# Kernel tuning notes

Hardware: AMD Instinct MI355X
Metric: run time of the kernel (lower is better)

## Reference

```python
import jax, jax.numpy as jnp
import numpy as np

B, K, D, H = 16, 256, 256, 128

def setup_inputs() -> dict:
    key = jax.random.key(0)
    k1, k2, k3 = jax.random.split(key, 3)
    x = jax.random.normal(k1, (B, K, D), dtype=jnp.float32)
    # Linear(2D, H): weight stored as (2D, H) for x @ W convention
    W1 = jax.random.normal(k2, (2 * D, H), dtype=jnp.float32) * (1.0 / np.sqrt(2 * D))
    b1 = jnp.zeros((H,), dtype=jnp.float32)
    W2 = jax.random.normal(k3, (H, D), dtype=jnp.float32) * (1.0 / np.sqrt(H))
    b2 = jnp.zeros((D,), dtype=jnp.float32)
    return {"x": x, "W1": W1, "b1": b1, "W2": W2, "b2": b2}

def reference(x, W1, b1, W2, b2):
    # Original: for each i, concat([x_i broadcast, x_j]) -> Linear -> ReLU -> Linear -> mean_j, + residual.
    # Split the first Linear over the concat: W1 = [W1a; W1b], so
    # pre-act(i,j) = x_i @ W1a + x_j @ W1b + b1  (avoids materializing the concat).
    D_ = x.shape[-1]
    W1a, W1b = W1[:D_], W1[D_:]
    a = jnp.einsum('bkd,dh->bkh', x, W1a)            # B x K x H (query side)
    b = jnp.einsum('bkd,dh->bkh', x, W1b)            # B x K x H (key side)
    h = jax.nn.relu(a[:, :, None, :] + b[:, None, :, :] + b1)  # B x K x K x H
    mh = h.mean(axis=2)                               # mean over j; Linear commutes with mean
    out = jnp.einsum('bkh,hd->bkd', mh, W2) + b2      # B x K x D
    return out + x
```

## Files before the change

kernel.cpp:

```cpp
#include <hip/hip_runtime.h>

typedef __attribute__((ext_vector_type(8))) short bf16x8;
typedef __attribute__((ext_vector_type(4))) float f32x4;

union FragU { uint4 q; bf16x8 h; };

__device__ __forceinline__ unsigned short f2bf(float f) {
  unsigned u = __float_as_uint(f);
  u += 0x7FFFu + ((u >> 16) & 1u);
  return (unsigned short)(u >> 16);
}
__device__ __forceinline__ unsigned pack2(float lo, float hi) {
  return (unsigned)f2bf(lo) | ((unsigned)f2bf(hi) << 16);
}

__global__ __launch_bounds__(256) void kX(
    const float* __restrict__ x, const float* __restrict__ W1,
    const float* __restrict__ W2, uint4* __restrict__ xbf,
    uint4* __restrict__ w1f, uint4* __restrict__ w2f)
{
  const int u = blockIdx.x * 256 + threadIdx.x;
  if (u < 131072) {
    const int l = u & 63, c = (u >> 6) & 7, t = (u >> 9) & 15, b = u >> 13;
    const int fr = l & 15, fq = l >> 4;
    const float* p = x + (size_t)((b * 16 + t) * 16 + fr) * 256 + c * 32 + fq * 8;
    float4 va = *(const float4*)p;
    float4 vb = *(const float4*)(p + 4);
    xbf[u] = make_uint4(pack2(va.x, va.y), pack2(va.z, va.w),
                        pack2(vb.x, vb.y), pack2(vb.z, vb.w));
  } else if (u < 139264) {
    const int u2 = u - 131072;
    const int l = u2 & 63, c = (u2 >> 6) & 7, hc = u2 >> 9;
    const int fr = l & 15, fq = l >> 4;
    const float* p = W1 + (size_t)((fr >= 8) ? 256 : 0) * 128 +
                     (size_t)(c * 32 + fq * 8) * 128 + hc * 8 + (fr & 7);
    float v[8];
#pragma unroll
    for (int j = 0; j < 8; ++j) v[j] = p[(size_t)j * 128];
    w1f[u2] = make_uint4(pack2(v[0], v[1]), pack2(v[2], v[3]),
                         pack2(v[4], v[5]), pack2(v[6], v[7]));
  } else if (u < 143360) {
    const int u3 = u - 139264;
    const int l = u3 & 63, c = (u3 >> 6) & 3, dg = u3 >> 8;
    const int fr = l & 15, fq = l >> 4;
    const float* p = W2 + (size_t)(c * 32 + fq * 8) * 256 + dg * 16 + fr;
    float v[8];
#pragma unroll
    for (int j = 0; j < 8; ++j) v[j] = p[(size_t)j * 256];
    w2f[u3] = make_uint4(pack2(v[0], v[1]), pack2(v[2], v[3]),
                         pack2(v[4], v[5]), pack2(v[6], v[7]));
  }
}

__global__ __launch_bounds__(1024) void kA(
    const uint4* __restrict__ xbf, const uint4* __restrict__ w1f,
    const float* __restrict__ b1, uint4* __restrict__ mf)
{
  __shared__ float Cs[8][260];
  __shared__ float As[8][260];
  __shared__ float sortedC[8][256];
  __shared__ float sufS[8][260];

  const int tid = threadIdx.x, lane = tid & 63, wv = tid >> 6;
  const int b = blockIdx.x, hc = blockIdx.y;
  const int fr = lane & 15, fq = lane >> 4;

  FragU afr[8];
#pragma unroll
  for (int c = 0; c < 8; ++c) afr[c].q = w1f[(hc * 8 + c) * 64 + lane];

  float b1v[4];
#pragma unroll
  for (int g = 0; g < 4; ++g)
    b1v[g] = (fq >= 2) ? b1[hc * 8 + (fq - 2) * 4 + g] : 0.f;

  {
    const int t = wv;
    f32x4 acc = {0.f, 0.f, 0.f, 0.f};
#pragma unroll
    for (int c = 0; c < 8; ++c) {
      FragU bfr;
      bfr.q = xbf[((size_t)(b * 16 + t) * 8 + c) * 64 + lane];
      acc = __builtin_amdgcn_mfma_f32_16x16x32_bf16(afr[c].h, bfr.h, acc, 0, 0, 0);
    }
    const int m = t * 16 + fr;
    if (fq < 2) {
#pragma unroll
      for (int g = 0; g < 4; ++g) As[fq * 4 + g][m] = acc[g];
    } else {
#pragma unroll
      for (int g = 0; g < 4; ++g) Cs[(fq - 2) * 4 + g][m] = acc[g] + b1v[g];
    }
  }
  __syncthreads();

  if (wv < 8) {
    const int hp = wv;
    float v0 = Cs[hp][lane * 4 + 0], v1 = Cs[hp][lane * 4 + 1];
    float v2 = Cs[hp][lane * 4 + 2], v3 = Cs[hp][lane * 4 + 3];

#define CE2(X, Y, UP)                                     \
    {                                                     \
      float mn = fminf(X, Y), mx = fmaxf(X, Y);           \
      X = (UP) ? mn : mx;  Y = (UP) ? mx : mn;            \
    }
    CE2(v0, v1, true) CE2(v2, v3, false)
    {
      const bool up4 = (lane & 1) == 0;
      CE2(v0, v2, up4) CE2(v1, v3, up4)
      CE2(v0, v1, up4) CE2(v2, v3, up4)
    }
#pragma unroll
    for (int k4 = 2; k4 <= 64; k4 <<= 1) {
      const bool up = (lane & k4) == 0;
#pragma unroll
      for (int j4 = k4 >> 1; j4 >= 1; j4 >>= 1) {
        const bool keepMin = (((lane & j4) == 0) == up);
#define CEX(V)                                            \
        {                                                 \
          float o = __shfl_xor(V, j4, 64);                \
          V = keepMin ? fminf(V, o) : fmaxf(V, o);        \
        }
        CEX(v0) CEX(v1) CEX(v2) CEX(v3)
#undef CEX
      }
      CE2(v0, v2, up) CE2(v1, v3, up)
      CE2(v0, v1, up) CE2(v2, v3, up)
    }
#undef CE2

    const float sl = (v0 + v1) + (v2 + v3);
    float inc = sl;
#pragma unroll
    for (int off = 1; off < 64; off <<= 1) {
      float t = __shfl_down(inc, off, 64);
      inc += (lane + off < 64) ? t : 0.f;
    }
    const float T = inc - sl;
    const float su3 = T + v3;
    const float su2 = su3 + v2;
    const float su1 = su2 + v1;
    const float su0 = su1 + v0;
    sortedC[hp][lane * 4 + 0] = v0;
    sortedC[hp][lane * 4 + 1] = v1;
    sortedC[hp][lane * 4 + 2] = v2;
    sortedC[hp][lane * 4 + 3] = v3;
    sufS[hp][lane * 4 + 0] = su0;
    sufS[hp][lane * 4 + 1] = su1;
    sufS[hp][lane * 4 + 2] = su2;
    sufS[hp][lane * 4 + 3] = su3;
    if (lane == 0) sufS[hp][256] = 0.f;
  }
  __syncthreads();

  {
    const int hp = wv & 7, half = wv >> 3;
#pragma unroll
    for (int q = 0; q < 2; ++q) {
      const int m = half * 128 + q * 64 + lane;
      const float a = As[hp][m];
      const float t = -a;
      int idx = 0;
#pragma unroll
      for (int st = 128; st >= 1; st >>= 1)
        idx += (sortedC[hp][idx + st - 1] <= t) ? st : 0;
      const float cnt = (float)(256 - idx);
      const float S = sufS[hp][idx];
      As[hp][m] = (cnt * a + S) * (1.f / 256.f);
    }
  }
  __syncthreads();

  if (tid < 256) {
    const int fr2 = tid & 15, T2 = tid >> 4;
    uint4 o = make_uint4(pack2(As[0][tid], As[1][tid]), pack2(As[2][tid], As[3][tid]),
                         pack2(As[4][tid], As[5][tid]), pack2(As[6][tid], As[7][tid]));
    mf[((size_t)(b * 16 + T2) * 4 + (hc >> 2)) * 64 + (hc & 3) * 16 + fr2] = o;
  }
}

__global__ __launch_bounds__(256) void kB(
    const uint4* __restrict__ mf, const uint4* __restrict__ w2f,
    const float* __restrict__ b2, const float* __restrict__ x,
    float* __restrict__ out)
{
  const int tid = threadIdx.x, lane = tid & 63, wu = tid >> 6;
  const int mt = blockIdx.x;
  const int dg = blockIdx.y * 4 + wu;
  const int fr = lane & 15, fq = lane >> 4;

  f32x4 acc = {0.f, 0.f, 0.f, 0.f};
#pragma unroll
  for (int c = 0; c < 4; ++c) {
    FragU a, bb;
    a.q  = mf[((size_t)mt * 4 + c) * 64 + lane];
    bb.q = w2f[((size_t)dg * 4 + c) * 64 + lane];
    acc = __builtin_amdgcn_mfma_f32_16x16x32_bf16(a.h, bb.h, acc, 0, 0, 0);
  }

  const int d = dg * 16 + fr;
  const float bv = b2[d];
#pragma unroll
  for (int g = 0; g < 4; ++g) {
    const int m = mt * 16 + fq * 4 + g;
    const size_t o = (size_t)m * 256 + d;
    out[o] = acc[g] + bv + x[o];
  }
}

extern "C" void kernel_launch(void* const* d_in, const int* in_sizes, int n_in,
                              void* d_out, int out_size, void* d_ws, size_t ws_size,
                              hipStream_t stream) {
  const float* x  = (const float*)d_in[0];
  const float* W1 = (const float*)d_in[1];
  const float* b1 = (const float*)d_in[2];
  const float* W2 = (const float*)d_in[3];
  const float* b2 = (const float*)d_in[4];
  float* out = (float*)d_out;

  char* ws = (char*)d_ws;
  uint4* xbf = (uint4*)ws;
  uint4* w1f = (uint4*)(ws + (2u << 20));
  uint4* w2f = (uint4*)(ws + (2u << 20) + (128u << 10));
  uint4* mf  = (uint4*)(ws + (2u << 20) + (192u << 10));

  kX<<<560, 256, 0, stream>>>(x, W1, W2, xbf, w1f, w2f);
  kA<<<dim3(16, 16), 1024, 0, stream>>>(xbf, w1f, b1, mf);
  kB<<<dim3(256, 4), 256, 0, stream>>>(mf, w2f, b2, x, out);
}
```

Measured before the change: 21.50 us.

## Replace per-element binary search with pivot count plus leaf scan in kA

In kA, the 8-step binary search over 256 sorted values and the full suffix-sum array are replaced by a two-level lookup. Each thread counts against 16 block pivots held in registers, reads one per-block suffix sum, then linearly scans a 16-element leaf in shared memory. kA also moves to 512 threads, with each wave doing two MFMA tiles and four queries, and every thread takes part in a narrower uint2 output write. kX and kB are relaunched with 1024-thread blocks, fewer of them, aiming to cut dependent LDS latency and launch/block overhead at the cost of more ALU compares per query.

```diff
diff --git a/kernel.cpp b/kernel.cpp
--- a/kernel.cpp
+++ b/kernel.cpp
@@ -14,12 +14,12 @@
   return (unsigned)f2bf(lo) | ((unsigned)f2bf(hi) << 16);
 }
 
-__global__ __launch_bounds__(256) void kX(
+__global__ __launch_bounds__(1024) void kX(
     const float* __restrict__ x, const float* __restrict__ W1,
     const float* __restrict__ W2, uint4* __restrict__ xbf,
     uint4* __restrict__ w1f, uint4* __restrict__ w2f)
 {
-  const int u = blockIdx.x * 256 + threadIdx.x;
+  const int u = blockIdx.x * 1024 + threadIdx.x;
   if (u < 131072) {
     const int l = u & 63, c = (u >> 6) & 7, t = (u >> 9) & 15, b = u >> 13;
     const int fr = l & 15, fq = l >> 4;
@@ -52,14 +52,15 @@
   }
 }
 
-__global__ __launch_bounds__(1024) void kA(
+__global__ __launch_bounds__(512) void kA(
     const uint4* __restrict__ xbf, const uint4* __restrict__ w1f,
     const float* __restrict__ b1, uint4* __restrict__ mf)
 {
   __shared__ float Cs[8][260];
   __shared__ float As[8][260];
   __shared__ float sortedC[8][256];
-  __shared__ float sufS[8][260];
+  __shared__ float Piv[8][16];
+  __shared__ float sufBlk[8][16];
 
   const int tid = threadIdx.x, lane = tid & 63, wv = tid >> 6;
   const int b = blockIdx.x, hc = blockIdx.y;
@@ -74,8 +75,9 @@
   for (int g = 0; g < 4; ++g)
     b1v[g] = (fq >= 2) ? b1[hc * 8 + (fq - 2) * 4 + g] : 0.f;
 
-  {
-    const int t = wv;
+#pragma unroll
+  for (int s = 0; s < 2; ++s) {
+    const int t = wv + s * 8;
     f32x4 acc = {0.f, 0.f, 0.f, 0.f};
 #pragma unroll
     for (int c = 0; c < 8; ++c) {
@@ -94,7 +96,7 @@
   }
   __syncthreads();
 
-  if (wv < 8) {
+  {
     const int hp = wv;
     float v0 = Cs[hp][lane * 4 + 0], v1 = Cs[hp][lane * 4 + 1];
     float v2 = Cs[hp][lane * 4 + 2], v3 = Cs[hp][lane * 4 + 3];
@@ -145,48 +147,64 @@
     sortedC[hp][lane * 4 + 1] = v1;
     sortedC[hp][lane * 4 + 2] = v2;
     sortedC[hp][lane * 4 + 3] = v3;
-    sufS[hp][lane * 4 + 0] = su0;
-    sufS[hp][lane * 4 + 1] = su1;
-    sufS[hp][lane * 4 + 2] = su2;
-    sufS[hp][lane * 4 + 3] = su3;
-    if (lane == 0) sufS[hp][256] = 0.f;
+    if ((lane & 3) == 3) Piv[hp][lane >> 2] = v3;
+    if ((lane & 3) == 0 && lane) sufBlk[hp][(lane >> 2) - 1] = su0;
+    if (lane == 0) sufBlk[hp][15] = 0.f;
   }
   __syncthreads();
 
   {
-    const int hp = wv & 7, half = wv >> 3;
-#pragma unroll
-    for (int q = 0; q < 2; ++q) {
-      const int m = half * 128 + q * 64 + lane;
+    const int hp = wv;
+    float piv[16];
+#pragma unroll
+    for (int j = 0; j < 16; j += 4) {
+      float4 pv = *(const float4*)&Piv[hp][j];
+      piv[j] = pv.x; piv[j + 1] = pv.y; piv[j + 2] = pv.z; piv[j + 3] = pv.w;
+    }
+#pragma unroll
+    for (int q = 0; q < 4; ++q) {
+      const int m = q * 64 + lane;
       const float a = As[hp][m];
       const float t = -a;
-      int idx = 0;
-#pragma unroll
-      for (int st = 128; st >= 1; st >>= 1)
-        idx += (sortedC[hp][idx + st - 1] <= t) ? st : 0;
-      const float cnt = (float)(256 - idx);
-      const float S = sufS[hp][idx];
-      As[hp][m] = (cnt * a + S) * (1.f / 256.f);
+      int p = 0;
+#pragma unroll
+      for (int j = 0; j < 16; ++j) p += (piv[j] <= t) ? 1 : 0;
+      p = (p > 15) ? 15 : p;
+      const float Sb = sufBlk[hp][p];
+      const float* leafp = &sortedC[hp][p * 16];
+      float sumL = 0.f; int cntL = 0;
+#pragma unroll
+      for (int j = 0; j < 16; j += 4) {
+        float4 lv = *(const float4*)&leafp[j];
+        if (lv.x > t) { sumL += lv.x; ++cntL; }
+        if (lv.y > t) { sumL += lv.y; ++cntL; }
+        if (lv.z > t) { sumL += lv.z; ++cntL; }
+        if (lv.w > t) { sumL += lv.w; ++cntL; }
+      }
+      const float cnt = (float)(240 - 16 * p + cntL);
+      As[hp][m] = (cnt * a + (Sb + sumL)) * (1.f / 256.f);
     }
   }
   __syncthreads();
 
-  if (tid < 256) {
-    const int fr2 = tid & 15, T2 = tid >> 4;
-    uint4 o = make_uint4(pack2(As[0][tid], As[1][tid]), pack2(As[2][tid], As[3][tid]),
-                         pack2(As[4][tid], As[5][tid]), pack2(As[6][tid], As[7][tid]));
-    mf[((size_t)(b * 16 + T2) * 4 + (hc >> 2)) * 64 + (hc & 3) * 16 + fr2] = o;
-  }
-}
-
-__global__ __launch_bounds__(256) void kB(
+  {
+    const int m = tid >> 1, half = tid & 1, j0 = half * 4;
+    const int fr2 = m & 15, T2 = m >> 4;
+    uint2 o = make_uint2(pack2(As[j0][m], As[j0 + 1][m]),
+                         pack2(As[j0 + 2][m], As[j0 + 3][m]));
+    const size_t unit = ((size_t)(b * 16 + T2) * 4 + (hc >> 2)) * 64 + (hc & 3) * 16 + fr2;
+    *(uint2*)((unsigned*)mf + unit * 4 + half * 2) = o;
+  }
+}
+
+__global__ __launch_bounds__(1024) void kB(
     const uint4* __restrict__ mf, const uint4* __restrict__ w2f,
     const float* __restrict__ b2, const float* __restrict__ x,
     float* __restrict__ out)
 {
   const int tid = threadIdx.x, lane = tid & 63, wu = tid >> 6;
   const int mt = blockIdx.x;
-  const int dg = blockIdx.y * 4 + wu;
+  const int dg = wu;
   const int fr = lane & 15, fq = lane >> 4;
 
   f32x4 acc = {0.f, 0.f, 0.f, 0.f};
@@ -224,7 +242,7 @@
   uint4* w2f = (uint4*)(ws + (2u << 20) + (128u << 10));
   uint4* mf  = (uint4*)(ws + (2u << 20) + (192u << 10));
 
-  kX<<<560, 256, 0, stream>>>(x, W1, W2, xbf, w1f, w2f);
-  kA<<<dim3(16, 16), 1024, 0, stream>>>(xbf, w1f, b1, mf);
-  kB<<<dim3(256, 4), 256, 0, stream>>>(mf, w2f, b2, x, out);
-}
+  kX<<<140, 1024, 0, stream>>>(x, W1, W2, xbf, w1f, w2f);
+  kA<<<dim3(16, 16), 512, 0, stream>>>(xbf, w1f, b1, mf);
+  kB<<<256, 1024, 0, stream>>>(mf, w2f, b2, x, out);
+}
```

Result: no change. 21.85 us (+1.6%).

## Fuse weight bf16 packing into consumers and split sort into two half-sorts

Applied to the files above, without the earlier changes.

Weight conversion to bf16 fragments moves out of the prep kernel and into kA and kB, which now read fp32 W1/W2 directly and pack them in registers. The sort of the C column now uses all 16 waves, each sorting 128 values. The ReLU-mean lookup becomes a two-level search (pivot count, then a 16-element leaf scan) across both sorted halves, replacing the binary search over one full sort. kB now runs one 1024-thread block per row tile. The aim is a shorter serial sort stage and less prep work, at the cost of redundant strided weight loads in every block.

```diff
diff --git a/kernel.cpp b/kernel.cpp
--- a/kernel.cpp
+++ b/kernel.cpp
@@ -14,60 +14,44 @@
   return (unsigned)f2bf(lo) | ((unsigned)f2bf(hi) << 16);
 }
 
-__global__ __launch_bounds__(256) void kX(
-    const float* __restrict__ x, const float* __restrict__ W1,
-    const float* __restrict__ W2, uint4* __restrict__ xbf,
-    uint4* __restrict__ w1f, uint4* __restrict__ w2f)
+__global__ __launch_bounds__(1024) void kX(
+    const float* __restrict__ x, uint4* __restrict__ xbf)
 {
-  const int u = blockIdx.x * 256 + threadIdx.x;
-  if (u < 131072) {
-    const int l = u & 63, c = (u >> 6) & 7, t = (u >> 9) & 15, b = u >> 13;
-    const int fr = l & 15, fq = l >> 4;
-    const float* p = x + (size_t)((b * 16 + t) * 16 + fr) * 256 + c * 32 + fq * 8;
-    float4 va = *(const float4*)p;
-    float4 vb = *(const float4*)(p + 4);
-    xbf[u] = make_uint4(pack2(va.x, va.y), pack2(va.z, va.w),
-                        pack2(vb.x, vb.y), pack2(vb.z, vb.w));
-  } else if (u < 139264) {
-    const int u2 = u - 131072;
-    const int l = u2 & 63, c = (u2 >> 6) & 7, hc = u2 >> 9;
-    const int fr = l & 15, fq = l >> 4;
-    const float* p = W1 + (size_t)((fr >= 8) ? 256 : 0) * 128 +
-                     (size_t)(c * 32 + fq * 8) * 128 + hc * 8 + (fr & 7);
-    float v[8];
-#pragma unroll
-    for (int j = 0; j < 8; ++j) v[j] = p[(size_t)j * 128];
-    w1f[u2] = make_uint4(pack2(v[0], v[1]), pack2(v[2], v[3]),
-                         pack2(v[4], v[5]), pack2(v[6], v[7]));
-  } else if (u < 143360) {
-    const int u3 = u - 139264;
-    const int l = u3 & 63, c = (u3 >> 6) & 3, dg = u3 >> 8;
-    const int fr = l & 15, fq = l >> 4;
-    const float* p = W2 + (size_t)(c * 32 + fq * 8) * 256 + dg * 16 + fr;
-    float v[8];
-#pragma unroll
-    for (int j = 0; j < 8; ++j) v[j] = p[(size_t)j * 256];
-    w2f[u3] = make_uint4(pack2(v[0], v[1]), pack2(v[2], v[3]),
-                         pack2(v[4], v[5]), pack2(v[6], v[7]));
-  }
+  const int u = blockIdx.x * 1024 + threadIdx.x;
+  const int l = u & 63, c = (u >> 6) & 7, t = (u >> 9) & 15, b = u >> 13;
+  const int fr = l & 15, fq = l >> 4;
+  const float* p = x + (size_t)((b * 16 + t) * 16 + fr) * 256 + c * 32 + fq * 8;
+  float4 va = *(const float4*)p;
+  float4 vb = *(const float4*)(p + 4);
+  xbf[u] = make_uint4(pack2(va.x, va.y), pack2(va.z, va.w),
+                      pack2(vb.x, vb.y), pack2(vb.z, vb.w));
 }
 
 __global__ __launch_bounds__(1024) void kA(
-    const uint4* __restrict__ xbf, const uint4* __restrict__ w1f,
+    const uint4* __restrict__ xbf, const float* __restrict__ W1,
     const float* __restrict__ b1, uint4* __restrict__ mf)
 {
   __shared__ float Cs[8][260];
   __shared__ float As[8][260];
   __shared__ float sortedC[8][256];
-  __shared__ float sufS[8][260];
+  __shared__ float Piv[8][16];
+  __shared__ float sufBlk[8][16];
 
   const int tid = threadIdx.x, lane = tid & 63, wv = tid >> 6;
   const int b = blockIdx.x, hc = blockIdx.y;
   const int fr = lane & 15, fq = lane >> 4;
 
+  const float* __restrict__ wp =
+      W1 + (size_t)((fr >= 8) ? 256 : 0) * 128 + hc * 8 + (fr & 7);
   FragU afr[8];
 #pragma unroll
-  for (int c = 0; c < 8; ++c) afr[c].q = w1f[(hc * 8 + c) * 64 + lane];
+  for (int c = 0; c < 8; ++c) {
+    float v[8];
+#pragma unroll
+    for (int j = 0; j < 8; ++j) v[j] = wp[(size_t)(c * 32 + fq * 8 + j) * 128];
+    afr[c].q = make_uint4(pack2(v[0], v[1]), pack2(v[2], v[3]),
+                          pack2(v[4], v[5]), pack2(v[6], v[7]));
+  }
 
   float b1v[4];
 #pragma unroll
@@ -94,42 +78,37 @@
   }
   __syncthreads();
 
-  if (wv < 8) {
-    const int hp = wv;
-    float v0 = Cs[hp][lane * 4 + 0], v1 = Cs[hp][lane * 4 + 1];
-    float v2 = Cs[hp][lane * 4 + 2], v3 = Cs[hp][lane * 4 + 3];
+  {
+    const int hp = wv & 7, half = wv >> 3;
+    const int base = half * 128;
+    float v0 = Cs[hp][base + lane * 2 + 0];
+    float v1 = Cs[hp][base + lane * 2 + 1];
 
 #define CE2(X, Y, UP)                                     \
     {                                                     \
       float mn = fminf(X, Y), mx = fmaxf(X, Y);           \
       X = (UP) ? mn : mx;  Y = (UP) ? mx : mn;            \
     }
-    CE2(v0, v1, true) CE2(v2, v3, false)
-    {
-      const bool up4 = (lane & 1) == 0;
-      CE2(v0, v2, up4) CE2(v1, v3, up4)
-      CE2(v0, v1, up4) CE2(v2, v3, up4)
-    }
-#pragma unroll
-    for (int k4 = 2; k4 <= 64; k4 <<= 1) {
-      const bool up = (lane & k4) == 0;
-#pragma unroll
-      for (int j4 = k4 >> 1; j4 >= 1; j4 >>= 1) {
-        const bool keepMin = (((lane & j4) == 0) == up);
+    { const bool up = (lane & 1) == 0; CE2(v0, v1, up) }
+#pragma unroll
+    for (int k2 = 2; k2 <= 64; k2 <<= 1) {
+      const bool up = (lane & k2) == 0;
+#pragma unroll
+      for (int j2 = k2 >> 1; j2 >= 1; j2 >>= 1) {
+        const bool keepMin = (((lane & j2) == 0) == up);
 #define CEX(V)                                            \
         {                                                 \
-          float o = __shfl_xor(V, j4, 64);                \
+          float o = __shfl_xor(V, j2, 64);                \
           V = keepMin ? fminf(V, o) : fmaxf(V, o);        \
         }
-        CEX(v0) CEX(v1) CEX(v2) CEX(v3)
+        CEX(v0) CEX(v1)
 #undef CEX
       }
-      CE2(v0, v2, up) CE2(v1, v3, up)
-      CE2(v0, v1, up) CE2(v2, v3, up)
+      CE2(v0, v1, up)
     }
 #undef CE2
 
-    const float sl = (v0 + v1) + (v2 + v3);
+    const float sl = v0 + v1;
     float inc = sl;
 #pragma unroll
     for (int off = 1; off < 64; off <<= 1) {
@@ -137,35 +116,58 @@
       inc += (lane + off < 64) ? t : 0.f;
     }
     const float T = inc - sl;
-    const float su3 = T + v3;
-    const float su2 = su3 + v2;
-    const float su1 = su2 + v1;
+    const float su1 = T + v1;
     const float su0 = su1 + v0;
-    sortedC[hp][lane * 4 + 0] = v0;
-    sortedC[hp][lane * 4 + 1] = v1;
-    sortedC[hp][lane * 4 + 2] = v2;
-    sortedC[hp][lane * 4 + 3] = v3;
-    sufS[hp][lane * 4 + 0] = su0;
-    sufS[hp][lane * 4 + 1] = su1;
-    sufS[hp][lane * 4 + 2] = su2;
-    sufS[hp][lane * 4 + 3] = su3;
-    if (lane == 0) sufS[hp][256] = 0.f;
+
+    sortedC[hp][base + lane * 2 + 0] = v0;
+    sortedC[hp][base + lane * 2 + 1] = v1;
+    if ((lane & 7) == 7) Piv[hp][half * 8 + (lane >> 3)] = v1;
+    if ((lane & 7) == 0 && lane) sufBlk[hp][half * 8 + (lane >> 3) - 1] = su0;
+    if (lane == 0) sufBlk[hp][half * 8 + 7] = 0.f;
   }
   __syncthreads();
 
   {
-    const int hp = wv & 7, half = wv >> 3;
+    const int hp = wv & 7, mq = wv >> 3;
+    float piv[16];
+#pragma unroll
+    for (int j = 0; j < 16; j += 4) {
+      float4 pv = *(const float4*)&Piv[hp][j];
+      piv[j] = pv.x; piv[j + 1] = pv.y; piv[j + 2] = pv.z; piv[j + 3] = pv.w;
+    }
 #pragma unroll
     for (int q = 0; q < 2; ++q) {
-      const int m = half * 128 + q * 64 + lane;
+      const int m = mq * 128 + q * 64 + lane;
       const float a = As[hp][m];
       const float t = -a;
-      int idx = 0;
-#pragma unroll
-      for (int st = 128; st >= 1; st >>= 1)
-        idx += (sortedC[hp][idx + st - 1] <= t) ? st : 0;
-      const float cnt = (float)(256 - idx);
-      const float S = sufS[hp][idx];
+      int p0 = 0, p1 = 0;
+#pragma unroll
+      for (int j = 0; j < 8; ++j) {
+        p0 += (piv[j] <= t) ? 1 : 0;
+        p1 += (piv[8 + j] <= t) ? 1 : 0;
+      }
+      p0 = (p0 > 7) ? 7 : p0;
+      p1 = (p1 > 7) ? 7 : p1;
+      const float Sb0 = sufBlk[hp][p0];
+      const float Sb1 = sufBlk[hp][8 + p1];
+      const float* leaf0 = &sortedC[hp][p0 * 16];
+      const float* leaf1 = &sortedC[hp][128 + p1 * 16];
+      float sum0 = 0.f, sum1 = 0.f; int cnt0 = 0, cnt1 = 0;
+#pragma unroll
+      for (int j = 0; j < 16; j += 4) {
+        float4 l0 = *(const float4*)&leaf0[j];
+        float4 l1 = *(const float4*)&leaf1[j];
+        if (l0.x > t) { sum0 += l0.x; ++cnt0; }
+        if (l0.y > t) { sum0 += l0.y; ++cnt0; }
+        if (l0.z > t) { sum0 += l0.z; ++cnt0; }
+        if (l0.w > t) { sum0 += l0.w; ++cnt0; }
+        if (l1.x > t) { sum1 += l1.x; ++cnt1; }
+        if (l1.y > t) { sum1 += l1.y; ++cnt1; }
+        if (l1.z > t) { sum1 += l1.z; ++cnt1; }
+        if (l1.w > t) { sum1 += l1.w; ++cnt1; }
+      }
+      const float cnt = (float)((112 - 16 * p0 + cnt0) + (112 - 16 * p1 + cnt1));
+      const float S = (Sb0 + sum0) + (Sb1 + sum1);
       As[hp][m] = (cnt * a + S) * (1.f / 256.f);
     }
   }
@@ -179,23 +181,33 @@
   }
 }
 
-__global__ __launch_bounds__(256) void kB(
-    const uint4* __restrict__ mf, const uint4* __restrict__ w2f,
+__global__ __launch_bounds__(1024) void kB(
+    const uint4* __restrict__ mf, const float* __restrict__ W2,
     const float* __restrict__ b2, const float* __restrict__ x,
     float* __restrict__ out)
 {
   const int tid = threadIdx.x, lane = tid & 63, wu = tid >> 6;
   const int mt = blockIdx.x;
-  const int dg = blockIdx.y * 4 + wu;
+  const int dg = wu;
   const int fr = lane & 15, fq = lane >> 4;
 
+  const float* __restrict__ w2p = W2 + dg * 16 + fr;
+  FragU bfr[4];
+#pragma unroll
+  for (int c = 0; c < 4; ++c) {
+    float v[8];
+#pragma unroll
+    for (int j = 0; j < 8; ++j) v[j] = w2p[(size_t)(c * 32 + fq * 8 + j) * 256];
+    bfr[c].q = make_uint4(pack2(v[0], v[1]), pack2(v[2], v[3]),
+                          pack2(v[4], v[5]), pack2(v[6], v[7]));
+  }
+
   f32x4 acc = {0.f, 0.f, 0.f, 0.f};
 #pragma unroll
   for (int c = 0; c < 4; ++c) {
-    FragU a, bb;
-    a.q  = mf[((size_t)mt * 4 + c) * 64 + lane];
-    bb.q = w2f[((size_t)dg * 4 + c) * 64 + lane];
-    acc = __builtin_amdgcn_mfma_f32_16x16x32_bf16(a.h, bb.h, acc, 0, 0, 0);
+    FragU a;
+    a.q = mf[((size_t)mt * 4 + c) * 64 + lane];
+    acc = __builtin_amdgcn_mfma_f32_16x16x32_bf16(a.h, bfr[c].h, acc, 0, 0, 0);
   }
 
   const int d = dg * 16 + fr;
@@ -220,11 +232,9 @@
 
   char* ws = (char*)d_ws;
   uint4* xbf = (uint4*)ws;
-  uint4* w1f = (uint4*)(ws + (2u << 20));
-  uint4* w2f = (uint4*)(ws + (2u << 20) + (128u << 10));
-  uint4* mf  = (uint4*)(ws + (2u << 20) + (192u << 10));
-
-  kX<<<560, 256, 0, stream>>>(x, W1, W2, xbf, w1f, w2f);
-  kA<<<dim3(16, 16), 1024, 0, stream>>>(xbf, w1f, b1, mf);
-  kB<<<dim3(256, 4), 256, 0, stream>>>(mf, w2f, b2, x, out);
-}
+  uint4* mf  = (uint4*)(ws + (2u << 20));
+
+  kX<<<128, 1024, 0, stream>>>(x, xbf);
+  kA<<<dim3(16, 16), 1024, 0, stream>>>(xbf, W1, b1, mf);
+  kB<<<256, 1024, 0, stream>>>(mf, W2, b2, x, out);
+}
```

After: 26.13 us. 1.22x slower.
